# Kernel tuning notes

Measured on AMD Instinct MI355X. Metric: run time of the kernel, lower is better.

## Reference

```python
import jax, jax.numpy as jnp
import numpy as np

F_DIM = 512
N_HEADS = 8
D_Q = 64
D_V = 64
EPS = 1e-6


def _xavier(key, shape):
    fan_in, fan_out = shape[0], shape[1]
    limit = float(np.sqrt(6.0 / (fan_in + fan_out)))
    return jax.random.uniform(key, shape, jnp.float32, -limit, limit)


def layer_norm(x, g, b):
    mu = jnp.mean(x, axis=-1, keepdims=True)
    var = jnp.mean(jnp.square(x - mu), axis=-1, keepdims=True)
    return (x - mu) * jax.lax.rsqrt(var + EPS) * g + b


def setup_inputs() -> dict:
    key = jax.random.key(0)
    ks = jax.random.split(key, 16)
    B, V, F = 4, 2048, F_DIM
    inp = {
        "texture_map1": jax.random.normal(ks[0], (B, V, F), jnp.float32),
        "texture_map2": jax.random.normal(ks[1], (B, V, F), jnp.float32),
        "ln1_g": jnp.ones((F,), jnp.float32), "ln1_b": jnp.zeros((F,), jnp.float32),
        "ln2_g": jnp.ones((F,), jnp.float32), "ln2_b": jnp.zeros((F,), jnp.float32),
        "Wq": _xavier(ks[2], (F, N_HEADS * D_Q)), "bq": jnp.zeros((N_HEADS * D_Q,), jnp.float32),
        "Wk": _xavier(ks[3], (F, N_HEADS * D_Q)), "bk": jnp.zeros((N_HEADS * D_Q,), jnp.float32),
        "Wv": _xavier(ks[4], (F, N_HEADS * D_V)), "bv": jnp.zeros((N_HEADS * D_V,), jnp.float32),
        "Wfc": _xavier(ks[5], (N_HEADS * D_V, F)), "bfc": jnp.zeros((F,), jnp.float32),
        "ff1_ln_g": jnp.ones((F,), jnp.float32), "ff1_ln_b": jnp.zeros((F,), jnp.float32),
        "ff1_W1": _xavier(ks[6], (F, F)), "ff1_b1": jnp.zeros((F,), jnp.float32),
        "ff1_W2": _xavier(ks[7], (F, F)), "ff1_b2": jnp.zeros((F,), jnp.float32),
        "ff2_ln_g": jnp.ones((F,), jnp.float32), "ff2_ln_b": jnp.zeros((F,), jnp.float32),
        "ff2_W1": _xavier(ks[8], (F, F)), "ff2_b1": jnp.zeros((F,), jnp.float32),
        "ff2_W2": _xavier(ks[9], (F, F)), "ff2_b2": jnp.zeros((F,), jnp.float32),
    }
    return inp


def _heads(x, d):
    B, V, _ = x.shape
    return x.reshape(B, V, N_HEADS, d).transpose(0, 2, 1, 3)  # [B,H,V,d]


def _ff_block(x, ln_g, ln_b, W1, b1, W2, b2):
    h = layer_norm(x, ln_g, ln_b)
    h = jax.nn.relu(h @ W1 + b1) @ W2 + b2
    return x + h


def reference(texture_map1, texture_map2, ln1_g, ln1_b, ln2_g, ln2_b,
              Wq, bq, Wk, bk, Wv, bv, Wfc, bfc,
              ff1_ln_g, ff1_ln_b, ff1_W1, ff1_b1, ff1_W2, ff1_b2,
              ff2_ln_g, ff2_ln_b, ff2_W1, ff2_b1, ff2_W2, ff2_b2):
    B, V, F = texture_map1.shape
    norm = D_Q ** 0.5
    t1n = layer_norm(texture_map1, ln1_g, ln1_b)
    t2n = layer_norm(texture_map2, ln2_g, ln2_b)
    q1 = _heads(t1n @ Wq + bq, D_Q)
    k1 = _heads(t1n @ Wk + bk, D_Q)
    v1 = _heads(t1n @ Wv + bv, D_V)
    q2 = _heads(t2n @ Wq + bq, D_Q)
    k2 = _heads(t2n @ Wk + bk, D_Q)
    v2 = _heads(t2n @ Wv + bv, D_V)
    # cross attention: 1 attends to 2, 2 attends to 1
    attn12 = jax.nn.softmax(jnp.einsum('bhqd,bhkd->bhqk', q1, k2) / norm, axis=-1)
    attn21 = jax.nn.softmax(jnp.einsum('bhqd,bhkd->bhqk', q2, k1) / norm, axis=-1)
    f12 = jnp.einsum('bhqk,bhkd->bhqd', attn12, v2).transpose(0, 2, 1, 3).reshape(B, V, -1)
    f21 = jnp.einsum('bhqk,bhkd->bhqd', attn21, v1).transpose(0, 2, 1, 3).reshape(B, V, -1)
    f12 = f12 @ Wfc + bfc
    f21 = f21 @ Wfc + bfc
    out1 = _ff_block(texture_map1 + f12, ff1_ln_g, ff1_ln_b, ff1_W1, ff1_b1, ff1_W2, ff1_b2)
    out2 = _ff_block(texture_map2 + f21, ff2_ln_g, ff2_ln_b, ff2_W1, ff2_b1, ff2_W2, ff2_b2)
    return (out1, out2)
```

## Files before the change

kernel.cpp:

```cpp
#include <hip/hip_runtime.h>
#include <stdint.h>

#define FD    512
#define SEQ   2048
#define NHALF 8192
#define NTOT  16384
#define QKVN  1536

typedef unsigned short u16;
typedef __attribute__((ext_vector_type(8))) short short8;
typedef __attribute__((ext_vector_type(4))) float f32x4;

__device__ __forceinline__ u16 f2bf(float f){
  union { float f; uint32_t i; } v; v.f = f;
  uint32_t r = v.i + 0x7FFFu + ((v.i >> 16) & 1u);
  return (u16)(r >> 16);
}

__device__ __forceinline__ float bf2f(u16 u){
  union { uint32_t i; float f; } v; v.i = ((uint32_t)u) << 16; return v.f;
}

__device__ __forceinline__ void gload_lds16(const void* g, void* l){
  __builtin_amdgcn_global_load_lds((const __attribute__((address_space(1))) void*)g,
                                   (__attribute__((address_space(3))) void*)l, 16, 0, 0);
}

__device__ __forceinline__ f32x4 mfma16(short8 a, short8 b, f32x4 c){
  return __builtin_amdgcn_mfma_f32_16x16x32_bf16(a, b, c, 0, 0, 0);
}

__device__ __forceinline__ uint32_t cvtpk(float lo, float hi){
  uint32_t r; asm("v_cvt_pk_bf16_f32 %0, %1, %2" : "=v"(r) : "v"(lo), "v"(hi)); return r;
}

__device__ __forceinline__ float fexp2(float x){
  float r; asm("v_exp_f32 %0, %1" : "=v"(r) : "v"(x)); return r;
}

__global__ __launch_bounds__(256) void wconv_kernel(
    const float* __restrict__ w0, const float* __restrict__ w1,
    const float* __restrict__ w2, const float* __restrict__ w3,
    const float* __restrict__ w4, const float* __restrict__ w5,
    const float* __restrict__ w6, const float* __restrict__ w7,
    u16* __restrict__ out)
{
  int mat = blockIdx.x >> 6;
  const float* w = w0;
  switch (mat){ case 1: w=w1; break; case 2: w=w2; break; case 3: w=w3; break;
                case 4: w=w4; break; case 5: w=w5; break; case 6: w=w6; break;
                case 7: w=w7; break; default: break; }
  int tile = blockIdx.x & 63;
  int k0 = (tile >> 3) << 6, n0 = (tile & 7) << 6;

  __shared__ float lt[64][65];
  int tid = threadIdx.x;
  int tr = tid >> 4, tc = (tid & 15) << 2;
  #pragma unroll
  for (int p = 0; p < 4; p++){
    int k = p * 16 + tr;
    float4 v = *(const float4*)&w[(size_t)(k0 + k) * 512 + n0 + tc];
    lt[k][tc] = v.x; lt[k][tc + 1] = v.y; lt[k][tc + 2] = v.z; lt[k][tc + 3] = v.w;
  }
  __syncthreads();
  int n = tid >> 2, kc = (tid & 3) << 4;
  u16 buf[16];
  #pragma unroll
  for (int j = 0; j < 16; j++) buf[j] = f2bf(lt[kc + j][n]);
  u16* dst = out + ((size_t)mat << 18) + (size_t)(n0 + n) * 512 + k0 + kc;
  *(short8*)dst       = *(const short8*)(buf);
  *(short8*)(dst + 8) = *(const short8*)(buf + 8);
}

__global__ __launch_bounds__(256) void biascat_kernel(
    const float* __restrict__ bq, const float* __restrict__ bk,
    const float* __restrict__ bv, float* __restrict__ o)
{
  int i = blockIdx.x * 256 + threadIdx.x;
  if (i < 512) o[i] = bq[i];
  else if (i < 1024) o[i] = bk[i - 512];
  else o[i] = bv[i - 1024];
}

template<bool INBF>
__global__ __launch_bounds__(256) void ln_kernel(
    const void* __restrict__ xa, const void* __restrict__ xb,
    const float* __restrict__ ga, const float* __restrict__ ba,
    const float* __restrict__ gb, const float* __restrict__ bb,
    u16* __restrict__ out)
{
  int row = (blockIdx.x << 2) + (threadIdx.x >> 6);
  int ln = threadIdx.x & 63;
  const void* xp; const float* g; const float* bi; int rl;
  if (row < NHALF){ xp = xa; g = ga; bi = ba; rl = row; }
  else            { xp = xb; g = gb; bi = bb; rl = row - NHALF; }
  int c = ln << 3;
  float d[8];
  if (INBF){
    short8 s8 = *(const short8*)((const u16*)xp + (size_t)rl * FD + c);
    #pragma unroll
    for (int j = 0; j < 8; j++) d[j] = bf2f((u16)s8[j]);
  } else {
    const float* x = (const float*)xp + (size_t)rl * FD + c;
    float4 v0 = *(const float4*)x;
    float4 v1 = *(const float4*)(x + 4);
    d[0]=v0.x; d[1]=v0.y; d[2]=v0.z; d[3]=v0.w;
    d[4]=v1.x; d[5]=v1.y; d[6]=v1.z; d[7]=v1.w;
  }
  float s = (d[0] + d[1]) + (d[2] + d[3]) + (d[4] + d[5]) + (d[6] + d[7]);
  #pragma unroll
  for (int o = 32; o; o >>= 1) s += __shfl_xor(s, o, 64);
  float mu = s * (1.0f / 512.0f);
  float q = 0.f;
  #pragma unroll
  for (int j = 0; j < 8; j++){ d[j] -= mu; q += d[j] * d[j]; }
  #pragma unroll
  for (int o = 32; o; o >>= 1) q += __shfl_xor(q, o, 64);
  float rs = rsqrtf(q * (1.0f / 512.0f) + 1e-6f);
  float4 g0 = *(const float4*)&g[c],  g1 = *(const float4*)&g[c + 4];
  float4 b0 = *(const float4*)&bi[c], b1 = *(const float4*)&bi[c + 4];
  float gg[8] = {g0.x, g0.y, g0.z, g0.w, g1.x, g1.y, g1.z, g1.w};
  float bbv[8] = {b0.x, b0.y, b0.z, b0.w, b1.x, b1.y, b1.z, b1.w};
  u16 o8[8];
  #pragma unroll
  for (int j = 0; j < 8; j++) o8[j] = f2bf(d[j] * rs * gg[j] + bbv[j]);
  *(short8*)&out[(size_t)row * FD + c] = *(const short8*)o8;
}

template<bool RELU, bool OUT_BF16, bool HAS_RES, bool RES_BF16, bool QKV_VT>
__global__ __launch_bounds__(256) void gemm_bt(
    const u16* __restrict__ A,
    const u16* __restrict__ BtLo, const u16* __restrict__ BtHi,
    const float* __restrict__ biasLo, const float* __restrict__ biasHi,
    const void* __restrict__ resLo, const void* __restrict__ resHi,
    void* __restrict__ outp, u16* __restrict__ vtp,
    int M, int N, int K, int halfM)
{
  __shared__ __align__(16) u16 lA[3][64 * 64];
  __shared__ __align__(16) u16 lB[3][64 * 64];
  int nwg = gridDim.x;
  int bid = (blockIdx.x & 7) * (nwg >> 3) + (blockIdx.x >> 3);
  int nTN = N >> 7;
  int bm = bid / nTN, bn = bid - bm * nTN;
  int rowBase = bm << 7, colBase = bn << 7;
  bool inLo = rowBase < halfM;
  const u16* Bt = inLo ? BtLo : BtHi;
  const float* bias = inLo ? biasLo : biasHi;
  const void* res = inLo ? resLo : resHi;
  int rowLocalBase = inLo ? rowBase : rowBase - halfM;

  int tid = threadIdx.x, wv = tid >> 6, ln = tid & 63;
  int g = ln >> 4, la = ln & 15;

  f32x4 acc[4][4];
  #pragma unroll
  for (int m = 0; m < 4; m++)
    #pragma unroll
    for (int n = 0; n < 4; n++) acc[m][n] = (f32x4){0.f, 0.f, 0.f, 0.f};

  int r   = tid >> 3;
  int sl  = (tid & 7) ^ (r & 7);
  int shalf = sl >> 2, sk8 = (sl & 3) << 3;
  const u16* gA0 = A  + (size_t)(rowBase + r + shalf * 64) * K + sk8;
  const u16* gB0 = Bt + (size_t)(colBase + r + shalf * 64) * K + sk8;
  const size_t row32 = (size_t)32 * K;

  int caA = (((wv >> 1) << 5) + (g << 3)) ^ ((la & 7) << 3);
  int caB = (((wv & 1) << 5) + (g << 3)) ^ ((la & 7) << 3);

  int arow = (wv >> 1) << 6, bcol = (wv & 1) << 6;

  #define STAGE(buf, kt) do { \
    gload_lds16(gA0 + (kt), (char*)lA[buf] + wv * 1024); \
    gload_lds16(gA0 + (kt) + row32, (char*)lA[buf] + 4096 + wv * 1024); \
    gload_lds16(gB0 + (kt), (char*)lB[buf] + wv * 1024); \
    gload_lds16(gB0 + (kt) + row32, (char*)lB[buf] + 4096 + wv * 1024); } while (0)

  int nK = K >> 5;
  STAGE(0, 0);
  STAGE(1, 32);

  for (int i = 0; i < nK; i++){
    if (i < nK - 1) asm volatile("s_waitcnt vmcnt(4)" ::: "memory");
    else            asm volatile("s_waitcnt vmcnt(0)" ::: "memory");
    __builtin_amdgcn_s_barrier();
    __builtin_amdgcn_sched_barrier(0);
    int cur = i % 3;
    if (i + 2 < nK) STAGE((i + 2) % 3, (i + 2) << 5);
    short8 af[4], bfr[4];
    #pragma unroll
    for (int m = 0; m < 4; m++)
      af[m] = *(const short8*)&lA[cur][((m << 4) + la) * 64 + caA];
    #pragma unroll
    for (int n = 0; n < 4; n++)
      bfr[n] = *(const short8*)&lB[cur][((n << 4) + la) * 64 + caB];
    #pragma unroll
    for (int m = 0; m < 4; m++)
      #pragma unroll
      for (int n = 0; n < 4; n++)
        acc[m][n] = mfma16(af[m], bfr[n], acc[m][n]);
  }
  #undef STAGE

  #pragma unroll
  for (int n = 0; n < 4; n++){
    int col = colBase + bcol + (n << 4) + la;
    float bv = bias[col];
    #pragma unroll
    for (int m = 0; m < 4; m++){
      int rowT = arow + (m << 4) + (g << 2);
      float v4[4];
      #pragma unroll
      for (int rr = 0; rr < 4; rr++){
        float v = acc[m][n][rr] + bv;
        if (RELU) v = fmaxf(v, 0.f);
        if (HAS_RES){
          size_t ri = (size_t)(rowLocalBase + rowT + rr) * N + col;
          if (RES_BF16) v += bf2f(((const u16*)res)[ri]);
          else          v += ((const float*)res)[ri];
        }
        v4[rr] = v;
      }
      if (QKV_VT && col >= 1024){
        int cv = col - 1024;
        int rowA = rowBase + rowT;
        int slab = ((rowA >= NHALF) ? 32 : 0) + (((rowA >> 11) & 3) << 3) + (cv >> 6);
        uint2 w; w.x = cvtpk(v4[0], v4[1]); w.y = cvtpk(v4[2], v4[3]);
        *(uint2*)&vtp[(size_t)slab * 131072 + (size_t)(cv & 63) * 2048 + (rowA & 2047)] = w;
      } else {
        #pragma unroll
        for (int rr = 0; rr < 4; rr++){
          if (OUT_BF16) ((u16*)outp)[(size_t)(rowBase + rowT + rr) * N + col] = f2bf(v4[rr]);
          else ((float*)outp)[(size_t)(rowBase + rowT + rr) * N + col] = v4[rr];
        }
      }
    }
  }
}

__global__ __launch_bounds__(512, 4) void attn_kernel(
    const u16* __restrict__ qkv, const u16* __restrict__ vt, u16* __restrict__ fb)
{
  int l = (blockIdx.x & 7) * 64 + (blockIdx.x >> 3);
  int qt = l & 7;
  int h  = (l >> 3) & 7;
  int z  = l >> 6;
  int dir = z >> 2, b = z & 3;
  int qRow0  = dir * NHALF + b * SEQ + qt * 256;
  int kvRow0 = (dir ^ 1) * NHALF + b * SEQ;
  int colQ = h * 64;

  __shared__ __align__(16) u16 lK[2][64 * 64];
  __shared__ __align__(16) u16 lVt[2][64 * 64];
  __shared__ __align__(16) u16 lP[8][32 * 64];

  int tid = threadIdx.x, wv = tid >> 6, ln = tid & 63;
  int g = ln >> 4, lo = ln & 15;

  int srow = tid >> 3;
  int soff = ((tid & 7) ^ (srow & 7)) * 8;

  const float CEXP = 0.18033688f;

  int ca0 = (g * 8) ^ ((lo & 7) << 3);
  int ca1 = (32 + g * 8) ^ ((lo & 7) << 3);
  int lo64 = lo * 64;

  int pidx[4];
  #pragma unroll
  for (int n = 0; n < 4; n++)
    pidx[n] = lo64 + ((n * 16 + g * 4) ^ ((lo & 7) << 3));
  int pra = lo64 + ca0, prb = lo64 + ca1;

  const u16* qbase  = qkv + (size_t)qRow0 * QKVN + colQ;
  const u16* vtbase = vt + (size_t)((dir ^ 1) * 32 + b * 8 + h) * 131072;

  const u16* kp0 = qkv + (size_t)(kvRow0 + srow) * QKVN + 512 + colQ + soff;
  const u16* vp0 = vtbase + (size_t)srow * 2048 + soff;

  char* dK0 = (char*)lK[0] + wv * 1024;
  char* dV0 = (char*)lVt[0] + wv * 1024;
  const u16* lKf = &lK[0][0];
  const u16* lVf = &lVt[0][0];
  u16* lPw = &lP[wv][0];

  gload_lds16(qbase + (size_t)srow * QKVN + soff,         (char*)lK[0]  + wv * 1024);
  gload_lds16(qbase + (size_t)(64 + srow) * QKVN + soff,  (char*)lK[1]  + wv * 1024);
  gload_lds16(qbase + (size_t)(128 + srow) * QKVN + soff, (char*)lVt[0] + wv * 1024);
  gload_lds16(qbase + (size_t)(192 + srow) * QKVN + soff, (char*)lVt[1] + wv * 1024);
  __syncthreads();
  const u16* qh;
  switch (wv >> 1){ case 0: qh = lK[0]; break; case 1: qh = lK[1]; break;
                    case 2: qh = lVt[0]; break; default: qh = lVt[1]; break; }
  int qr0 = (wv & 1) * 32 + lo;
  short8 qf00 = *(const short8*)&qh[qr0 * 64 + ca0];
  short8 qf01 = *(const short8*)&qh[qr0 * 64 + ca1];
  short8 qf10 = *(const short8*)&qh[(qr0 + 16) * 64 + ca0];
  short8 qf11 = *(const short8*)&qh[(qr0 + 16) * 64 + ca1];
  __syncthreads();

  gload_lds16(kp0, dK0);
  gload_lds16(vp0, dV0);
  kp0 += (size_t)64 * QKVN; vp0 += 64;
  __syncthreads();

  f32x4 acc_o0[4], acc_o1[4];
  #pragma unroll
  for (int nd = 0; nd < 4; nd++){
    acc_o0[nd] = (f32x4){0.f, 0.f, 0.f, 0.f};
    acc_o1[nd] = (f32x4){0.f, 0.f, 0.f, 0.f};
  }
  f32x4 acc_l0 = (f32x4){0.f, 0.f, 0.f, 0.f};
  f32x4 acc_l1 = (f32x4){0.f, 0.f, 0.f, 0.f};
  float m_l0, m_l1;
  const f32x4 z4 = (f32x4){0.f, 0.f, 0.f, 0.f};

  short8 ones;
  #pragma unroll
  for (int j = 0; j < 8; j++) ones[j] = (short)0x3F80;

  int cb = 0;
  for (int t = 0; t < 32; t++){
    if (t < 31){
      int nb = cb ^ 8192;
      gload_lds16(kp0, dK0 + nb);
      gload_lds16(vp0, dV0 + nb);
      kp0 += (size_t)64 * QKVN; vp0 += 64;
    }
    const u16* lk = (const u16*)((const char*)lKf + cb);
    const u16* lv = (const u16*)((const char*)lVf + cb);

    f32x4 s0[4], s1[4];
    #pragma unroll
    for (int n = 0; n < 4; n++){
      short8 kfa = *(const short8*)&lk[lo64 + n * 1024 + ca0];
      short8 kfb = *(const short8*)&lk[lo64 + n * 1024 + ca1];
      s0[n] = mfma16(kfa, qf00, z4);
      s0[n] = mfma16(kfb, qf01, s0[n]);
      s1[n] = mfma16(kfa, qf10, z4);
      s1[n] = mfma16(kfb, qf11, s1[n]);
    }

    float m00, m01;
    {
      float t0 = fmaxf(fmaxf(s0[0][0], s0[0][1]), fmaxf(s0[0][2], s0[0][3]));
      float t1 = fmaxf(fmaxf(s0[1][0], s0[1][1]), fmaxf(s0[1][2], s0[1][3]));
      float t2 = fmaxf(fmaxf(s0[2][0], s0[2][1]), fmaxf(s0[2][2], s0[2][3]));
      float t3 = fmaxf(fmaxf(s0[3][0], s0[3][1]), fmaxf(s0[3][2], s0[3][3]));
      m00 = fmaxf(fmaxf(t0, t1), fmaxf(t2, t3));
      m00 = fmaxf(m00, __shfl_xor(m00, 16, 64));
      m00 = fmaxf(m00, __shfl_xor(m00, 32, 64));
      m00 *= CEXP;
    }
    {
      float t0 = fmaxf(fmaxf(s1[0][0], s1[0][1]), fmaxf(s1[0][2], s1[0][3]));
      float t1 = fmaxf(fmaxf(s1[1][0], s1[1][1]), fmaxf(s1[1][2], s1[1][3]));
      float t2 = fmaxf(fmaxf(s1[2][0], s1[2][1]), fmaxf(s1[2][2], s1[2][3]));
      float t3 = fmaxf(fmaxf(s1[3][0], s1[3][1]), fmaxf(s1[3][2], s1[3][3]));
      m01 = fmaxf(fmaxf(t0, t1), fmaxf(t2, t3));
      m01 = fmaxf(m01, __shfl_xor(m01, 16, 64));
      m01 = fmaxf(m01, __shfl_xor(m01, 32, 64));
      m01 *= CEXP;
    }

    if (t == 0){ m_l0 = m00; m_l1 = m01; }

    #pragma unroll
    for (int n = 0; n < 4; n++){
      float p0 = fexp2(fmaf(s0[n][0], CEXP, -m_l0));
      float p1 = fexp2(fmaf(s0[n][1], CEXP, -m_l0));
      float p2 = fexp2(fmaf(s0[n][2], CEXP, -m_l0));
      float p3 = fexp2(fmaf(s0[n][3], CEXP, -m_l0));
      uint2 pk0; pk0.x = cvtpk(p0, p1); pk0.y = cvtpk(p2, p3);
      *(uint2*)&lPw[pidx[n]] = pk0;
      float q0 = fexp2(fmaf(s1[n][0], CEXP, -m_l1));
      float q1 = fexp2(fmaf(s1[n][1], CEXP, -m_l1));
      float q2 = fexp2(fmaf(s1[n][2], CEXP, -m_l1));
      float q3 = fexp2(fmaf(s1[n][3], CEXP, -m_l1));
      uint2 pk1; pk1.x = cvtpk(q0, q1); pk1.y = cvtpk(q2, q3);
      *(uint2*)&lPw[pidx[n] + 1024] = pk1;
    }

    short8 pf00 = *(const short8*)&lPw[pra];
    short8 pf01 = *(const short8*)&lPw[prb];
    short8 pf10 = *(const short8*)&lPw[pra + 1024];
    short8 pf11 = *(const short8*)&lPw[prb + 1024];
    acc_l0 = mfma16(pf00, ones, acc_l0);
    acc_l0 = mfma16(pf01, ones, acc_l0);
    acc_l1 = mfma16(pf10, ones, acc_l1);
    acc_l1 = mfma16(pf11, ones, acc_l1);
    #pragma unroll
    for (int nd = 0; nd < 4; nd++){
      short8 vfa = *(const short8*)&lv[lo64 + nd * 1024 + ca0];
      short8 vfb = *(const short8*)&lv[lo64 + nd * 1024 + ca1];
      acc_o0[nd] = mfma16(pf00, vfa, acc_o0[nd]);
      acc_o0[nd] = mfma16(pf01, vfb, acc_o0[nd]);
      acc_o1[nd] = mfma16(pf10, vfa, acc_o1[nd]);
      acc_o1[nd] = mfma16(pf11, vfb, acc_o1[nd]);
    }

    bool ok = (m00 <= m_l0 + 8.f) && (m01 <= m_l1 + 8.f);
    if (!__all(ok)){
      float mn0 = fmaxf(m_l0, m00);
      float mn1 = fmaxf(m_l1, m01);
      float a00 = fexp2(m_l0 - mn0);
      float a01 = fexp2(m_l1 - mn1);
      m_l0 = mn0; m_l1 = mn1;
      #pragma unroll
      for (int r = 0; r < 4; r++){
        float ar0 = __shfl(a00, g * 4 + r, 64);
        float ar1 = __shfl(a01, g * 4 + r, 64);
        acc_l0[r] *= ar0;
        acc_l1[r] *= ar1;
        #pragma unroll
        for (int nd = 0; nd < 4; nd++){
          acc_o0[nd][r] *= ar0;
          acc_o1[nd][r] *= ar1;
        }
      }
    }

    cb ^= 8192;
    __syncthreads();
  }

  #pragma unroll
  for (int r = 0; r < 4; r++){
    float rl0 = 1.0f / acc_l0[r];
    float rl1 = 1.0f / acc_l1[r];
    #pragma unroll
    for (int nd = 0; nd < 4; nd++){
      int row0 = qRow0 + wv * 32 + g * 4 + r;
      int d    = colQ + (nd << 4) + lo;
      fb[(size_t)row0 * FD + d]        = f2bf(acc_o0[nd][r] * rl0);
      fb[(size_t)(row0 + 16) * FD + d] = f2bf(acc_o1[nd][r] * rl1);
    }
  }
}

extern "C" void kernel_launch(void* const* d_in, const int* in_sizes, int n_in,
                              void* d_out, int out_size, void* d_ws, size_t ws_size,
                              hipStream_t stream)
{
  const float* t1   = (const float*)d_in[0];
  const float* t2   = (const float*)d_in[1];
  const float* ln1g = (const float*)d_in[2];
  const float* ln1b = (const float*)d_in[3];
  const float* ln2g = (const float*)d_in[4];
  const float* ln2b = (const float*)d_in[5];
  const float* Wq   = (const float*)d_in[6];
  const float* bq   = (const float*)d_in[7];
  const float* Wk   = (const float*)d_in[8];
  const float* bk   = (const float*)d_in[9];
  const float* Wv   = (const float*)d_in[10];
  const float* bv   = (const float*)d_in[11];
  const float* Wfc  = (const float*)d_in[12];
  const float* bfc  = (const float*)d_in[13];
  const float* f1lg = (const float*)d_in[14];
  const float* f1lb = (const float*)d_in[15];
  const float* W11  = (const float*)d_in[16];
  const float* b11  = (const float*)d_in[17];
  const float* W12  = (const float*)d_in[18];
  const float* b12  = (const float*)d_in[19];
  const float* f2lg = (const float*)d_in[20];
  const float* f2lb = (const float*)d_in[21];
  const float* W21  = (const float*)d_in[22];
  const float* b21  = (const float*)d_in[23];
  const float* W22  = (const float*)d_in[24];
  const float* b22  = (const float*)d_in[25];

  char* ws = (char*)d_ws;
  const size_t MB = 1024 * 1024;
  u16* wt     = (u16*)ws;
  u16* tln    = (u16*)(ws + 4 * MB);
  u16* qkv    = (u16*)(ws + 20 * MB);
  u16* fb     = (u16*)(ws + 68 * MB);
  float* bqkv = (float*)(ws + 84 * MB);
  u16* vtb    = (u16*)(ws + 85 * MB);
  u16* xln    = tln;
  u16* hb     = qkv;
  u16* xb     = (u16*)(ws + 36 * MB);
  float* out  = (float*)d_out;

  wconv_kernel<<<512, 256, 0, stream>>>(Wq, Wk, Wv, Wfc, W11, W12, W21, W22, wt);
  biascat_kernel<<<6, 256, 0, stream>>>(bq, bk, bv, bqkv);
  ln_kernel<false><<<4096, 256, 0, stream>>>(t1, t2, ln1g, ln1b, ln2g, ln2b, tln);
  gemm_bt<false, true, false, false, true><<<1536, 256, 0, stream>>>(
      tln, wt, wt, bqkv, bqkv, nullptr, nullptr, qkv, vtb, NTOT, QKVN, FD, NTOT);
  attn_kernel<<<512, 512, 0, stream>>>(qkv, vtb, fb);
  gemm_bt<false, true, true, false, false><<<512, 256, 0, stream>>>(
      fb, wt + 3 * 262144, wt + 3 * 262144, bfc, bfc, t1, t2, xb, nullptr, NTOT, FD, FD, NHALF);
  ln_kernel<true><<<4096, 256, 0, stream>>>(xb, xb + (size_t)NHALF * FD,
      f1lg, f1lb, f2lg, f2lb, xln);
  gemm_bt<true, true, false, false, false><<<512, 256, 0, stream>>>(
      xln, wt + 4 * 262144, wt + 6 * 262144, b11, b21, nullptr, nullptr, hb, nullptr, NTOT, FD, FD, NHALF);
  gemm_bt<false, false, true, true, false><<<512, 256, 0, stream>>>(
      hb, wt + 5 * 262144, wt + 7 * 262144, b12, b22, xb, xb + (size_t)NHALF * FD,
      out, nullptr, NTOT, FD, FD, NHALF);
}
```

Before: 210.0 us.

## Rewrite attention with 32x32 MFMA and register-resident P via permlane swaps

Attention now uses 32x32x16 bf16 MFMA tiles instead of 16x16x32. The softmax probabilities are repacked in registers with v_permlane32_swap rather than written to and re-read from an LDS scratch buffer, so the per-warp P buffer is removed. Q is loaded straight from global memory into registers, and the row sum is accumulated with scalar adds instead of an extra MFMA against a ones vector. The aim is to cut LDS traffic and MFMA issue count, at the cost of more register pressure and a new fragment-layout mapping that must be exactly right.

```diff
diff --git a/kernel.cpp b/kernel.cpp
--- a/kernel.cpp
+++ b/kernel.cpp
@@ -10,6 +10,7 @@
 typedef unsigned short u16;
 typedef __attribute__((ext_vector_type(8))) short short8;
 typedef __attribute__((ext_vector_type(4))) float f32x4;
+typedef __attribute__((ext_vector_type(16))) float f32x16;
 
 __device__ __forceinline__ u16 f2bf(float f){
   union { float f; uint32_t i; } v; v.f = f;
@@ -30,8 +31,16 @@
   return __builtin_amdgcn_mfma_f32_16x16x32_bf16(a, b, c, 0, 0, 0);
 }
 
+__device__ __forceinline__ f32x16 mfma32(short8 a, short8 b, f32x16 c){
+  return __builtin_amdgcn_mfma_f32_32x32x16_bf16(a, b, c, 0, 0, 0);
+}
+
 __device__ __forceinline__ uint32_t cvtpk(float lo, float hi){
   uint32_t r; asm("v_cvt_pk_bf16_f32 %0, %1, %2" : "=v"(r) : "v"(lo), "v"(hi)); return r;
+}
+
+__device__ __forceinline__ void plswap(uint32_t &a, uint32_t &b){
+  asm volatile("v_permlane32_swap_b32 %0, %1" : "+v"(a), "+v"(b));
 }
 
 __device__ __forceinline__ float fexp2(float x){
@@ -241,10 +250,10 @@
 __global__ __launch_bounds__(512, 4) void attn_kernel(
     const u16* __restrict__ qkv, const u16* __restrict__ vt, u16* __restrict__ fb)
 {
-  int l = (blockIdx.x & 7) * 64 + (blockIdx.x >> 3);
-  int qt = l & 7;
-  int h  = (l >> 3) & 7;
-  int z  = l >> 6;
+  int l_ = (blockIdx.x & 7) * 64 + (blockIdx.x >> 3);
+  int qt = l_ & 7;
+  int h  = (l_ >> 3) & 7;
+  int z  = l_ >> 6;
   int dir = z >> 2, b = z & 3;
   int qRow0  = dir * NHALF + b * SEQ + qt * 256;
   int kvRow0 = (dir ^ 1) * NHALF + b * SEQ;
@@ -252,29 +261,24 @@
 
   __shared__ __align__(16) u16 lK[2][64 * 64];
   __shared__ __align__(16) u16 lVt[2][64 * 64];
-  __shared__ __align__(16) u16 lP[8][32 * 64];
 
   int tid = threadIdx.x, wv = tid >> 6, ln = tid & 63;
-  int g = ln >> 4, lo = ln & 15;
+  int q5 = ln & 31, hi = ln >> 5;
 
   int srow = tid >> 3;
   int soff = ((tid & 7) ^ (srow & 7)) * 8;
 
   const float CEXP = 0.18033688f;
 
-  int ca0 = (g * 8) ^ ((lo & 7) << 3);
-  int ca1 = (32 + g * 8) ^ ((lo & 7) << 3);
-  int lo64 = lo * 64;
-
-  int pidx[4];
-  #pragma unroll
-  for (int n = 0; n < 4; n++)
-    pidx[n] = lo64 + ((n * 16 + g * 4) ^ ((lo & 7) << 3));
-  int pra = lo64 + ca0, prb = lo64 + ca1;
-
-  const u16* qbase  = qkv + (size_t)qRow0 * QKVN + colQ;
+  int fsw = (q5 & 7) << 3;
+  int fidx[2][4];
+  #pragma unroll
+  for (int blk = 0; blk < 2; blk++)
+    #pragma unroll
+    for (int ks = 0; ks < 4; ks++)
+      fidx[blk][ks] = (blk * 32 + q5) * 64 + ((ks * 16 + hi * 8) ^ fsw);
+
   const u16* vtbase = vt + (size_t)((dir ^ 1) * 32 + b * 8 + h) * 131072;
-
   const u16* kp0 = qkv + (size_t)(kvRow0 + srow) * QKVN + 512 + colQ + soff;
   const u16* vp0 = vtbase + (size_t)srow * 2048 + soff;
 
@@ -282,42 +286,23 @@
   char* dV0 = (char*)lVt[0] + wv * 1024;
   const u16* lKf = &lK[0][0];
   const u16* lVf = &lVt[0][0];
-  u16* lPw = &lP[wv][0];
-
-  gload_lds16(qbase + (size_t)srow * QKVN + soff,         (char*)lK[0]  + wv * 1024);
-  gload_lds16(qbase + (size_t)(64 + srow) * QKVN + soff,  (char*)lK[1]  + wv * 1024);
-  gload_lds16(qbase + (size_t)(128 + srow) * QKVN + soff, (char*)lVt[0] + wv * 1024);
-  gload_lds16(qbase + (size_t)(192 + srow) * QKVN + soff, (char*)lVt[1] + wv * 1024);
-  __syncthreads();
-  const u16* qh;
-  switch (wv >> 1){ case 0: qh = lK[0]; break; case 1: qh = lK[1]; break;
-                    case 2: qh = lVt[0]; break; default: qh = lVt[1]; break; }
-  int qr0 = (wv & 1) * 32 + lo;
-  short8 qf00 = *(const short8*)&qh[qr0 * 64 + ca0];
-  short8 qf01 = *(const short8*)&qh[qr0 * 64 + ca1];
-  short8 qf10 = *(const short8*)&qh[(qr0 + 16) * 64 + ca0];
-  short8 qf11 = *(const short8*)&qh[(qr0 + 16) * 64 + ca1];
-  __syncthreads();
+
+  const u16* qp = qkv + (size_t)(qRow0 + wv * 32 + q5) * QKVN + colQ + hi * 8;
+  short8 qf0 = *(const short8*)(qp);
+  short8 qf1 = *(const short8*)(qp + 16);
+  short8 qf2 = *(const short8*)(qp + 32);
+  short8 qf3 = *(const short8*)(qp + 48);
 
   gload_lds16(kp0, dK0);
   gload_lds16(vp0, dV0);
   kp0 += (size_t)64 * QKVN; vp0 += 64;
   __syncthreads();
 
-  f32x4 acc_o0[4], acc_o1[4];
-  #pragma unroll
-  for (int nd = 0; nd < 4; nd++){
-    acc_o0[nd] = (f32x4){0.f, 0.f, 0.f, 0.f};
-    acc_o1[nd] = (f32x4){0.f, 0.f, 0.f, 0.f};
-  }
-  f32x4 acc_l0 = (f32x4){0.f, 0.f, 0.f, 0.f};
-  f32x4 acc_l1 = (f32x4){0.f, 0.f, 0.f, 0.f};
-  float m_l0, m_l1;
-  const f32x4 z4 = (f32x4){0.f, 0.f, 0.f, 0.f};
-
-  short8 ones;
-  #pragma unroll
-  for (int j = 0; j < 8; j++) ones[j] = (short)0x3F80;
+  f32x16 acc0, acc1;
+  #pragma unroll
+  for (int j = 0; j < 16; j++){ acc0[j] = 0.f; acc1[j] = 0.f; }
+  float acc_ls = 0.f;
+  float m_l = 0.f;
 
   int cb = 0;
   for (int t = 0; t < 32; t++){
@@ -330,93 +315,73 @@
     const u16* lk = (const u16*)((const char*)lKf + cb);
     const u16* lv = (const u16*)((const char*)lVf + cb);
 
-    f32x4 s0[4], s1[4];
-    #pragma unroll
-    for (int n = 0; n < 4; n++){
-      short8 kfa = *(const short8*)&lk[lo64 + n * 1024 + ca0];
-      short8 kfb = *(const short8*)&lk[lo64 + n * 1024 + ca1];
-      s0[n] = mfma16(kfa, qf00, z4);
-      s0[n] = mfma16(kfb, qf01, s0[n]);
-      s1[n] = mfma16(kfa, qf10, z4);
-      s1[n] = mfma16(kfb, qf11, s1[n]);
+    f32x16 s0, s1;
+    s0 = mfma32(*(const short8*)&lk[fidx[0][0]], qf0, acc0 * 0.f);
+    s0 = mfma32(*(const short8*)&lk[fidx[0][1]], qf1, s0);
+    s0 = mfma32(*(const short8*)&lk[fidx[0][2]], qf2, s0);
+    s0 = mfma32(*(const short8*)&lk[fidx[0][3]], qf3, s0);
+    s1 = mfma32(*(const short8*)&lk[fidx[1][0]], qf0, acc0 * 0.f);
+    s1 = mfma32(*(const short8*)&lk[fidx[1][1]], qf1, s1);
+    s1 = mfma32(*(const short8*)&lk[fidx[1][2]], qf2, s1);
+    s1 = mfma32(*(const short8*)&lk[fidx[1][3]], qf3, s1);
+
+    float m0;
+    {
+      float a0 = fmaxf(fmaxf(s0[0], s0[1]), fmaxf(s0[2], s0[3]));
+      float a1 = fmaxf(fmaxf(s0[4], s0[5]), fmaxf(s0[6], s0[7]));
+      float a2 = fmaxf(fmaxf(s0[8], s0[9]), fmaxf(s0[10], s0[11]));
+      float a3 = fmaxf(fmaxf(s0[12], s0[13]), fmaxf(s0[14], s0[15]));
+      float b0 = fmaxf(fmaxf(s1[0], s1[1]), fmaxf(s1[2], s1[3]));
+      float b1 = fmaxf(fmaxf(s1[4], s1[5]), fmaxf(s1[6], s1[7]));
+      float b2 = fmaxf(fmaxf(s1[8], s1[9]), fmaxf(s1[10], s1[11]));
+      float b3 = fmaxf(fmaxf(s1[12], s1[13]), fmaxf(s1[14], s1[15]));
+      m0 = fmaxf(fmaxf(fmaxf(a0, a1), fmaxf(a2, a3)),
+                 fmaxf(fmaxf(b0, b1), fmaxf(b2, b3)));
+      m0 = fmaxf(m0, __shfl_xor(m0, 32, 64));
+      m0 *= CEXP;
     }
-
-    float m00, m01;
-    {
-      float t0 = fmaxf(fmaxf(s0[0][0], s0[0][1]), fmaxf(s0[0][2], s0[0][3]));
-      float t1 = fmaxf(fmaxf(s0[1][0], s0[1][1]), fmaxf(s0[1][2], s0[1][3]));
-      float t2 = fmaxf(fmaxf(s0[2][0], s0[2][1]), fmaxf(s0[2][2], s0[2][3]));
-      float t3 = fmaxf(fmaxf(s0[3][0], s0[3][1]), fmaxf(s0[3][2], s0[3][3]));
-      m00 = fmaxf(fmaxf(t0, t1), fmaxf(t2, t3));
-      m00 = fmaxf(m00, __shfl_xor(m00, 16, 64));
-      m00 = fmaxf(m00, __shfl_xor(m00, 32, 64));
-      m00 *= CEXP;
-    }
-    {
-      float t0 = fmaxf(fmaxf(s1[0][0], s1[0][1]), fmaxf(s1[0][2], s1[0][3]));
-      float t1 = fmaxf(fmaxf(s1[1][0], s1[1][1]), fmaxf(s1[1][2], s1[1][3]));
-      float t2 = fmaxf(fmaxf(s1[2][0], s1[2][1]), fmaxf(s1[2][2], s1[2][3]));
-      float t3 = fmaxf(fmaxf(s1[3][0], s1[3][1]), fmaxf(s1[3][2], s1[3][3]));
-      m01 = fmaxf(fmaxf(t0, t1), fmaxf(t2, t3));
-      m01 = fmaxf(m01, __shfl_xor(m01, 16, 64));
-      m01 = fmaxf(m01, __shfl_xor(m01, 32, 64));
-      m01 *= CEXP;
-    }
-
-    if (t == 0){ m_l0 = m00; m_l1 = m01; }
-
-    #pragma unroll
-    for (int n = 0; n < 4; n++){
-      float p0 = fexp2(fmaf(s0[n][0], CEXP, -m_l0));
-      float p1 = fexp2(fmaf(s0[n][1], CEXP, -m_l0));
-      float p2 = fexp2(fmaf(s0[n][2], CEXP, -m_l0));
-      float p3 = fexp2(fmaf(s0[n][3], CEXP, -m_l0));
-      uint2 pk0; pk0.x = cvtpk(p0, p1); pk0.y = cvtpk(p2, p3);
-      *(uint2*)&lPw[pidx[n]] = pk0;
-      float q0 = fexp2(fmaf(s1[n][0], CEXP, -m_l1));
-      float q1 = fexp2(fmaf(s1[n][1], CEXP, -m_l1));
-      float q2 = fexp2(fmaf(s1[n][2], CEXP, -m_l1));
-      float q3 = fexp2(fmaf(s1[n][3], CEXP, -m_l1));
-      uint2 pk1; pk1.x = cvtpk(q0, q1); pk1.y = cvtpk(q2, q3);
-      *(uint2*)&lPw[pidx[n] + 1024] = pk1;
-    }
-
-    short8 pf00 = *(const short8*)&lPw[pra];
-    short8 pf01 = *(const short8*)&lPw[prb];
-    short8 pf10 = *(const short8*)&lPw[pra + 1024];
-    short8 pf11 = *(const short8*)&lPw[prb + 1024];
-    acc_l0 = mfma16(pf00, ones, acc_l0);
-    acc_l0 = mfma16(pf01, ones, acc_l0);
-    acc_l1 = mfma16(pf10, ones, acc_l1);
-    acc_l1 = mfma16(pf11, ones, acc_l1);
-    #pragma unroll
-    for (int nd = 0; nd < 4; nd++){
-      short8 vfa = *(const short8*)&lv[lo64 + nd * 1024 + ca0];
-      short8 vfb = *(const short8*)&lv[lo64 + nd * 1024 + ca1];
-      acc_o0[nd] = mfma16(pf00, vfa, acc_o0[nd]);
-      acc_o0[nd] = mfma16(pf01, vfb, acc_o0[nd]);
-      acc_o1[nd] = mfma16(pf10, vfa, acc_o1[nd]);
-      acc_o1[nd] = mfma16(pf11, vfb, acc_o1[nd]);
-    }
-
-    bool ok = (m00 <= m_l0 + 8.f) && (m01 <= m_l1 + 8.f);
-    if (!__all(ok)){
-      float mn0 = fmaxf(m_l0, m00);
-      float mn1 = fmaxf(m_l1, m01);
-      float a00 = fexp2(m_l0 - mn0);
-      float a01 = fexp2(m_l1 - mn1);
-      m_l0 = mn0; m_l1 = mn1;
+    if (t == 0) m_l = m0;
+
+    float ps = 0.f;
+    #define PKB(SK, KS0, KS1) do { \
+      float p[16]; \
+      _Pragma("unroll") \
+      for (int j = 0; j < 16; j++){ p[j] = fexp2(fmaf(SK[j], CEXP, -m_l)); ps += p[j]; } \
+      uint32_t A0 = cvtpk(p[0], p[1]),  A1 = cvtpk(p[2], p[3]); \
+      uint32_t B0 = cvtpk(p[4], p[5]),  B1 = cvtpk(p[6], p[7]); \
+      uint32_t C0 = cvtpk(p[8], p[9]),  C1 = cvtpk(p[10], p[11]); \
+      uint32_t D0 = cvtpk(p[12], p[13]), D1 = cvtpk(p[14], p[15]); \
+      plswap(A0, B0); plswap(A1, B1); \
+      plswap(C0, D0); plswap(C1, D1); \
+      union { uint32_t u[4]; short8 s8; } fa, fb_; \
+      fa.u[0] = A0; fa.u[1] = A1; fa.u[2] = B0; fa.u[3] = B1; \
+      fb_.u[0] = C0; fb_.u[1] = C1; fb_.u[2] = D0; fb_.u[3] = D1; \
+      short8 vA0 = *(const short8*)&lv[fidx[0][KS0]]; \
+      short8 vA1 = *(const short8*)&lv[fidx[1][KS0]]; \
+      short8 vB0 = *(const short8*)&lv[fidx[0][KS1]]; \
+      short8 vB1 = *(const short8*)&lv[fidx[1][KS1]]; \
+      acc0 = mfma32(fa.s8, vA0, acc0); \
+      acc1 = mfma32(fa.s8, vA1, acc1); \
+      acc0 = mfma32(fb_.s8, vB0, acc0); \
+      acc1 = mfma32(fb_.s8, vB1, acc1); \
+    } while (0)
+
+    PKB(s0, 0, 1);
+    PKB(s1, 2, 3);
+    #undef PKB
+    acc_ls += ps;
+
+    if (!__all(m0 <= m_l + 8.f)){
+      float mn = fmaxf(m_l, m0);
+      float a0 = fexp2(m_l - mn);
+      m_l = mn;
+      acc_ls *= a0;
       #pragma unroll
-      for (int r = 0; r < 4; r++){
-        float ar0 = __shfl(a00, g * 4 + r, 64);
-        float ar1 = __shfl(a01, g * 4 + r, 64);
-        acc_l0[r] *= ar0;
-        acc_l1[r] *= ar1;
-        #pragma unroll
-        for (int nd = 0; nd < 4; nd++){
-          acc_o0[nd][r] *= ar0;
-          acc_o1[nd][r] *= ar1;
-        }
+      for (int reg = 0; reg < 16; reg++){
+        int qr = (reg & 3) + 8 * (reg >> 2) + 4 * hi;
+        float ar = __shfl(a0, qr, 64);
+        acc0[reg] *= ar;
+        acc1[reg] *= ar;
       }
     }
 
@@ -424,17 +389,15 @@
     __syncthreads();
   }
 
-  #pragma unroll
-  for (int r = 0; r < 4; r++){
-    float rl0 = 1.0f / acc_l0[r];
-    float rl1 = 1.0f / acc_l1[r];
-    #pragma unroll
-    for (int nd = 0; nd < 4; nd++){
-      int row0 = qRow0 + wv * 32 + g * 4 + r;
-      int d    = colQ + (nd << 4) + lo;
-      fb[(size_t)row0 * FD + d]        = f2bf(acc_o0[nd][r] * rl0);
-      fb[(size_t)(row0 + 16) * FD + d] = f2bf(acc_o1[nd][r] * rl1);
-    }
+  float lsum = acc_ls + __shfl_xor(acc_ls, 32, 64);
+  float rcp = 1.0f / lsum;
+  #pragma unroll
+  for (int reg = 0; reg < 16; reg++){
+    int qr = (reg & 3) + 8 * (reg >> 2) + 4 * hi;
+    float rl = __shfl(rcp, qr, 64);
+    size_t row = (size_t)(qRow0 + wv * 32 + qr) * FD + colQ + q5;
+    fb[row]      = f2bf(acc0[reg] * rl);
+    fb[row + 32] = f2bf(acc1[reg] * rl);
   }
 }
 
@@ -474,7 +437,7 @@
   u16* wt     = (u16*)ws;
   u16* tln    = (u16*)(ws + 4 * MB);
   u16* qkv    = (u16*)(ws + 20 * MB);
-  u16* fb     = (u16*)(ws + 68 * MB);
+  u16* fbuf   = (u16*)(ws + 68 * MB);
   float* bqkv = (float*)(ws + 84 * MB);
   u16* vtb    = (u16*)(ws + 85 * MB);
   u16* xln    = tln;
@@ -487,9 +450,9 @@
   ln_kernel<false><<<4096, 256, 0, stream>>>(t1, t2, ln1g, ln1b, ln2g, ln2b, tln);
   gemm_bt<false, true, false, false, true><<<1536, 256, 0, stream>>>(
       tln, wt, wt, bqkv, bqkv, nullptr, nullptr, qkv, vtb, NTOT, QKVN, FD, NTOT);
-  attn_kernel<<<512, 512, 0, stream>>>(qkv, vtb, fb);
+  attn_kernel<<<512, 512, 0, stream>>>(qkv, vtb, fbuf);
   gemm_bt<false, true, true, false, false><<<512, 256, 0, stream>>>(
-      fb, wt + 3 * 262144, wt + 3 * 262144, bfc, bfc, t1, t2, xb, nullptr, NTOT, FD, FD, NHALF);
+      fbuf, wt + 3 * 262144, wt + 3 * 262144, bfc, bfc, t1, t2, xb, nullptr, NTOT, FD, FD, NHALF);
   ln_kernel<true><<<4096, 256, 0, stream>>>(xb, xb + (size_t)NHALF * FD,
       f1lg, f1lb, f2lg, f2lb, xln);
   gemm_bt<true, true, false, false, false><<<512, 256, 0, stream>>>(
```

After: 210.5 us. Within noise of the previous version (+0.2%).
